# Optimization experiments

Hardware: AMD Instinct MI355X
Metric: run time of the kernel (lower is better)

The kernel has to match this reference:

```python
import jax, jax.numpy as jnp
import numpy as np
from jax import lax

B, N, H = 2048, 8192, 10  # batch, grid points, MLP hidden width (default NetworkStructure)
BETA = 0.1                # G(x) = 1 - exp(-beta*x)


def setup_inputs() -> dict:
    key = jax.random.key(0)
    ks = jax.random.split(key, 12)
    y_plus = jax.random.uniform(ks[0], (B, 1), dtype=jnp.float32) * 500.0
    i = jax.random.randint(ks[1], (B, 1), 0, N)
    DU_DY = jax.random.normal(ks[2], (B, 1, N), dtype=jnp.float32)
    # Y is a strictly increasing wall-normal grid per sample
    incr = jax.random.uniform(ks[3], (B, 1, N), dtype=jnp.float32) * 0.01 + 1e-4
    Y = jnp.cumsum(incr, axis=-1)
    s = 0.3
    # alphanet MLP (1 -> H -> 1)
    aw1 = jax.random.normal(ks[4], (1, H), dtype=jnp.float32) * s
    ab1 = jax.random.normal(ks[5], (H,), dtype=jnp.float32) * s
    aw2 = jax.random.normal(ks[6], (H, 1), dtype=jnp.float32) * s
    ab2 = jax.random.normal(ks[7], (1,), dtype=jnp.float32) * s
    # output MLP (1 -> H -> 1)
    w1 = jax.random.normal(ks[8], (1, H), dtype=jnp.float32) * s
    b1 = jax.random.normal(ks[9], (H,), dtype=jnp.float32) * s
    w2 = jax.random.normal(ks[10], (H, 1), dtype=jnp.float32) * s
    b2 = jax.random.normal(ks[11], (1,), dtype=jnp.float32) * s
    return {"y_plus": y_plus, "i": i, "DU_DY": DU_DY, "Y": Y,
            "aw1": aw1, "ab1": ab1, "aw2": aw2, "ab2": ab2,
            "w1": w1, "b1": b1, "w2": w2, "b2": b2}


def _mlp(x, w1, b1, w2, b2):
    return jax.nn.relu(x @ w1 + b1) @ w2 + b2


def _d_alpha_u(a, n, du, y):
    """Vectorized Caputo-style fractional derivative.
    a: [B] alpha in [0,1]; n: [B] int index; du, y: [B, N]."""
    yn = jnp.take_along_axis(y, n[:, None], axis=1)[:, 0]            # Y[n]
    t = (1.0 - a)[:, None]                                            # exponent 1-alpha
    k = jnp.arange(y.shape[1])
    mask = k[None, :] <= (n[:, None] - 2)                             # k = 0 .. n-2
    y_next = jnp.concatenate([y[:, 1:], y[:, -1:]], axis=1)          # Y[k+1]
    d0 = jnp.where(mask, yn[:, None] - y, 1.0)                        # guard neg bases
    d1 = jnp.where(mask, yn[:, None] - y_next, 1.0)
    bk = jnp.where(mask, d0 ** t - d1 ** t, 0.0)
    sum_main = jnp.sum(bk * du, axis=1)
    nm1 = jnp.clip(n - 1, 0)
    y_nm1 = jnp.take_along_axis(y, nm1[:, None], axis=1)[:, 0]
    du_nm1 = jnp.take_along_axis(du, nm1[:, None], axis=1)[:, 0]
    base = jnp.where(n >= 1, yn - y_nm1, 1.0)
    last = jnp.where(n >= 1, base ** t[:, 0] * du_nm1, 0.0)
    fac = jnp.exp(-lax.lgamma(2.0 - a))                               # 1/Gamma(2-a)
    frac = jnp.where(n == 0, 0.0, fac * (sum_main + last))
    # alpha == 0 branch: trapezoid integral of DU_DY up to index n
    seg = (y[:, 1:] - y[:, :-1]) * (du[:, 1:] + du[:, :-1]) * 0.5
    cum = jnp.concatenate([jnp.zeros((y.shape[0], 1), y.dtype), jnp.cumsum(seg, axis=1)], axis=1)
    trap = jnp.take_along_axis(cum, n[:, None], axis=1)[:, 0]
    # alpha == 1 branch: DU_DY[n]
    dun = jnp.take_along_axis(du, n[:, None], axis=1)[:, 0]
    return jnp.where(a == 0.0, trap, jnp.where(a == 1.0, dun, frac))


def reference(y_plus, i, DU_DY, Y, aw1, ab1, aw2, ab2, w1, b1, w2, b2):
    # AlphaNet with alpha0=1: alpha = 1 - sigmoid(mlp(y+)) * (1 - exp(-beta*y+))
    g = 1.0 - jnp.exp(-BETA * y_plus)
    alpha = 1.0 - jax.nn.sigmoid(_mlp(y_plus, aw1, ab1, aw2, ab2)) * g   # [B,1]
    a = alpha[:, 0]
    n = i[:, 0]
    du = DU_DY[:, 0, :]
    y = Y[:, 0, :]
    d = _d_alpha_u(a, n, du, y)[:, None]                                  # [B,1]
    return _mlp(d, w1, b1, w2, b2)
```

## Files before the change

kernel.cpp:

```cpp
#include <hip/hip_runtime.h>
#include <math.h>

#define BB 2048
#define NN 8192
#define HH 10
#define BETA 0.1f

__device__ __forceinline__ float fast_log2(float x) {
    float r; asm("v_log_f32 %0, %1" : "=v"(r) : "v"(x)); return r;
}
__device__ __forceinline__ float fast_exp2(float x) {
    float r; asm("v_exp_f32 %0, %1" : "=v"(r) : "v"(x)); return r;
}

__global__ __launch_bounds__(256) void frac_mlp_kernel(
    const float* __restrict__ y_plus,
    const int*   __restrict__ iidx,
    const float* __restrict__ DU,
    const float* __restrict__ Y,
    const float* __restrict__ aw1, const float* __restrict__ ab1,
    const float* __restrict__ aw2, const float* __restrict__ ab2,
    const float* __restrict__ w1,  const float* __restrict__ b1,
    const float* __restrict__ w2,  const float* __restrict__ b2,
    float* __restrict__ out)
{
    const int b   = blockIdx.x;
    const int tid = threadIdx.x;
    const int n   = iidx[b];
    const float yp = y_plus[b];

    float m = ab2[0];
    #pragma unroll
    for (int h = 0; h < HH; ++h)
        m += fmaxf(fmaf(yp, aw1[h], ab1[h]), 0.f) * aw2[h];
    const float g   = 1.f - expf(-BETA * yp);
    const float sig = 1.f / (1.f + expf(-m));
    const float a   = 1.f - sig * g;
    const float t   = 1.f - a;

    const float* yr = Y  + (size_t)b * NN;
    const float* dr = DU + (size_t)b * NN;
    const float yn = yr[n];

    double sm = 0.0;
    double tr = 0.0;

    const bool need_main = (a != 0.f) && (a != 1.f) && (n >= 2);
    const bool need_trap = (a == 0.f) && (n >= 1);

    if (need_main) {
        const int kend = n - 2;
        for (int k0 = tid * 8; k0 <= kend; k0 += 256 * 8) {
            float4 ya = *reinterpret_cast<const float4*>(yr + k0);
            float4 yb = *reinterpret_cast<const float4*>(yr + k0 + 4);
            float4 da = *reinterpret_cast<const float4*>(dr + k0);
            float4 db = *reinterpret_cast<const float4*>(dr + k0 + 4);
            float ynext = (k0 + 8 <= kend + 1) ? yr[k0 + 8] : yb.w;
            float yv[9] = {ya.x, ya.y, ya.z, ya.w, yb.x, yb.y, yb.z, yb.w, ynext};
            float dv[8] = {da.x, da.y, da.z, da.w, db.x, db.y, db.z, db.w};
            float p[9];
            #pragma unroll
            for (int j = 0; j < 9; ++j) {
                float x = fmaxf(yn - yv[j], 1e-30f);
                p[j] = fast_exp2(t * fast_log2(x));
            }
            float acc = 0.f;
            #pragma unroll
            for (int q = 0; q < 8; ++q) {
                if (k0 + q <= kend)
                    acc = fmaf(p[q] - p[q + 1], dv[q], acc);
            }
            sm += (double)acc;
        }
    }
    if (need_trap) {
        const int kend = n - 1;
        for (int k0 = tid * 4; k0 <= kend; k0 += 256 * 4) {
            float4 y4 = *reinterpret_cast<const float4*>(yr + k0);
            float4 d4 = *reinterpret_cast<const float4*>(dr + k0);
            float ynext = (k0 + 4 <= kend + 1) ? yr[k0 + 4] : y4.w;
            float dnext = (k0 + 4 <= kend + 1) ? dr[k0 + 4] : d4.w;
            float yv[5] = {y4.x, y4.y, y4.z, y4.w, ynext};
            float dv[5] = {d4.x, d4.y, d4.z, d4.w, dnext};
            float acc = 0.f;
            #pragma unroll
            for (int q = 0; q < 4; ++q) {
                int k = k0 + q;
                if (k <= kend)
                    acc += (yv[q + 1] - yv[q]) * (dv[q + 1] + dv[q]) * 0.5f;
            }
            tr += (double)acc;
        }
    }

    for (int off = 32; off > 0; off >>= 1) {
        sm += __shfl_down(sm, off, 64);
        tr += __shfl_down(tr, off, 64);
    }
    __shared__ double s_sm[4], s_tr[4];
    const int wave = tid >> 6, lane = tid & 63;
    if (lane == 0) { s_sm[wave] = sm; s_tr[wave] = tr; }
    __syncthreads();

    if (tid == 0) {
        double smT = s_sm[0] + s_sm[1] + s_sm[2] + s_sm[3];
        double trT = s_tr[0] + s_tr[1] + s_tr[2] + s_tr[3];
        float dres;
        if (a == 0.f) {
            dres = (float)trT;
        } else if (a == 1.f) {
            dres = dr[n];
        } else if (n == 0) {
            dres = 0.f;
        } else {
            float last = powf(yn - yr[n - 1], t) * dr[n - 1];
            float fac  = expf(-lgammaf(2.f - a));
            dres = fac * ((float)smT + last);
        }
        float o = b2[0];
        #pragma unroll
        for (int h = 0; h < HH; ++h)
            o += fmaxf(fmaf(dres, w1[h], b1[h]), 0.f) * w2[h];
        out[b] = o;
    }
}

extern "C" void kernel_launch(void* const* d_in, const int* in_sizes, int n_in,
                              void* d_out, int out_size, void* d_ws, size_t ws_size,
                              hipStream_t stream) {
    const float* y_plus = (const float*)d_in[0];
    const int*   iidx   = (const int*)  d_in[1];
    const float* DU     = (const float*)d_in[2];
    const float* Y      = (const float*)d_in[3];
    const float* aw1    = (const float*)d_in[4];
    const float* ab1    = (const float*)d_in[5];
    const float* aw2    = (const float*)d_in[6];
    const float* ab2    = (const float*)d_in[7];
    const float* w1     = (const float*)d_in[8];
    const float* b1     = (const float*)d_in[9];
    const float* w2     = (const float*)d_in[10];
    const float* b2     = (const float*)d_in[11];
    float* out = (float*)d_out;

    frac_mlp_kernel<<<BB, 256, 0, stream>>>(y_plus, iidx, DU, Y,
                                            aw1, ab1, aw2, ab2,
                                            w1, b1, w2, b2, out);
}
```

Baseline: 18.73 us.

## Split per-sample reduction across four blocks with a separate finalize kernel

Each sample's sum over up to 8192 grid points is now split across four blocks (a 2D grid). Each thread handles exactly one 8-element chunk and writes a double partial to workspace. A second small kernel adds the partials and runs the final MLP per sample. The aim is more parallelism and shorter per-block latency, at the cost of a second launch, workspace traffic, and blocks whose chunk lies past n and exit with almost no work.

```diff
diff --git a/kernel.cpp b/kernel.cpp
--- a/kernel.cpp
+++ b/kernel.cpp
@@ -5,6 +5,8 @@
 #define NN 8192
 #define HH 10
 #define BETA 0.1f
+#define CHUNK 2048
+#define NSPLIT 4
 
 __device__ __forceinline__ float fast_log2(float x) {
     float r; asm("v_log_f32 %0, %1" : "=v"(r) : "v"(x)); return r;
@@ -13,7 +15,105 @@
     float r; asm("v_exp_f32 %0, %1" : "=v"(r) : "v"(x)); return r;
 }
 
-__global__ __launch_bounds__(256) void frac_mlp_kernel(
+__device__ __forceinline__ float alpha_of(float yp,
+    const float* __restrict__ aw1, const float* __restrict__ ab1,
+    const float* __restrict__ aw2, const float* __restrict__ ab2) {
+    float m = ab2[0];
+    #pragma unroll
+    for (int h = 0; h < HH; ++h)
+        m += fmaxf(fmaf(yp, aw1[h], ab1[h]), 0.f) * aw2[h];
+    const float g   = 1.f - expf(-BETA * yp);
+    const float sig = 1.f / (1.f + expf(-m));
+    return 1.f - sig * g;
+}
+
+__global__ __launch_bounds__(256) void frac_partial_kernel(
+    const float* __restrict__ y_plus,
+    const int*   __restrict__ iidx,
+    const float* __restrict__ DU,
+    const float* __restrict__ Y,
+    const float* __restrict__ aw1, const float* __restrict__ ab1,
+    const float* __restrict__ aw2, const float* __restrict__ ab2,
+    double2* __restrict__ ws2)
+{
+    const int b   = blockIdx.x;
+    const int s   = blockIdx.y;
+    const int tid = threadIdx.x;
+    const int n   = iidx[b];
+
+    const float a = alpha_of(y_plus[b], aw1, ab1, aw2, ab2);
+    const float t = 1.f - a;
+
+    const float* yr = Y  + (size_t)b * NN;
+    const float* dr = DU + (size_t)b * NN;
+
+    const bool need_main = (a != 0.f) && (a != 1.f) && (n >= 2);
+    const bool need_trap = (a == 0.f) && (n >= 1);
+
+    float sm = 0.f;
+    float tr = 0.f;
+
+    if (need_main) {
+        const int kend = n - 2;
+        const int k0 = s * CHUNK + tid * 8;
+        if (k0 <= kend) {
+            float4 ya = *reinterpret_cast<const float4*>(yr + k0);
+            float4 yb = *reinterpret_cast<const float4*>(yr + k0 + 4);
+            float4 da = *reinterpret_cast<const float4*>(dr + k0);
+            float4 db = *reinterpret_cast<const float4*>(dr + k0 + 4);
+            float ynext = (k0 + 8 <= kend + 1) ? yr[k0 + 8] : yb.w;
+            const float yn = yr[n];
+            float yv[9] = {ya.x, ya.y, ya.z, ya.w, yb.x, yb.y, yb.z, yb.w, ynext};
+            float dv[8] = {da.x, da.y, da.z, da.w, db.x, db.y, db.z, db.w};
+            float p[9];
+            #pragma unroll
+            for (int j = 0; j < 9; ++j) {
+                float x = fmaxf(yn - yv[j], 1e-30f);
+                p[j] = fast_exp2(t * fast_log2(x));
+            }
+            #pragma unroll
+            for (int q = 0; q < 8; ++q)
+                if (k0 + q <= kend)
+                    sm = fmaf(p[q] - p[q + 1], dv[q], sm);
+        }
+    }
+    if (need_trap) {
+        const int kend = n - 1;
+        const int k0 = s * CHUNK + tid * 8;
+        if (k0 <= kend) {
+            float4 ya = *reinterpret_cast<const float4*>(yr + k0);
+            float4 yb = *reinterpret_cast<const float4*>(yr + k0 + 4);
+            float4 da = *reinterpret_cast<const float4*>(dr + k0);
+            float4 db = *reinterpret_cast<const float4*>(dr + k0 + 4);
+            float ynext = (k0 + 8 <= kend + 1) ? yr[k0 + 8] : yb.w;
+            float dnext = (k0 + 8 <= kend + 1) ? dr[k0 + 8] : db.w;
+            float yv[9] = {ya.x, ya.y, ya.z, ya.w, yb.x, yb.y, yb.z, yb.w, ynext};
+            float dv[9] = {da.x, da.y, da.z, da.w, db.x, db.y, db.z, db.w, dnext};
+            #pragma unroll
+            for (int q = 0; q < 8; ++q)
+                if (k0 + q <= kend)
+                    tr += (yv[q + 1] - yv[q]) * (dv[q + 1] + dv[q]) * 0.5f;
+        }
+    }
+
+    double smd = (double)sm, trd = (double)tr;
+    for (int off = 32; off > 0; off >>= 1) {
+        smd += __shfl_down(smd, off, 64);
+        trd += __shfl_down(trd, off, 64);
+    }
+    __shared__ double s_sm[4], s_tr[4];
+    const int wave = tid >> 6, lane = tid & 63;
+    if (lane == 0) { s_sm[wave] = smd; s_tr[wave] = trd; }
+    __syncthreads();
+    if (tid == 0) {
+        double2 r;
+        r.x = s_sm[0] + s_sm[1] + s_sm[2] + s_sm[3];
+        r.y = s_tr[0] + s_tr[1] + s_tr[2] + s_tr[3];
+        ws2[b * NSPLIT + s] = r;
+    }
+}
+
+__global__ __launch_bounds__(256) void frac_final_kernel(
     const float* __restrict__ y_plus,
     const int*   __restrict__ iidx,
     const float* __restrict__ DU,
@@ -22,107 +122,42 @@
     const float* __restrict__ aw2, const float* __restrict__ ab2,
     const float* __restrict__ w1,  const float* __restrict__ b1,
     const float* __restrict__ w2,  const float* __restrict__ b2,
+    const double2* __restrict__ ws2,
     float* __restrict__ out)
 {
-    const int b   = blockIdx.x;
-    const int tid = threadIdx.x;
-    const int n   = iidx[b];
-    const float yp = y_plus[b];
+    const int b = blockIdx.x * 256 + threadIdx.x;
+    if (b >= BB) return;
+    const int n = iidx[b];
+    const float a = alpha_of(y_plus[b], aw1, ab1, aw2, ab2);
+    const float t = 1.f - a;
 
-    float m = ab2[0];
+    double sm = 0.0, tr = 0.0;
     #pragma unroll
-    for (int h = 0; h < HH; ++h)
-        m += fmaxf(fmaf(yp, aw1[h], ab1[h]), 0.f) * aw2[h];
-    const float g   = 1.f - expf(-BETA * yp);
-    const float sig = 1.f / (1.f + expf(-m));
-    const float a   = 1.f - sig * g;
-    const float t   = 1.f - a;
+    for (int s = 0; s < NSPLIT; ++s) {
+        double2 r = ws2[b * NSPLIT + s];
+        sm += r.x; tr += r.y;
+    }
 
     const float* yr = Y  + (size_t)b * NN;
     const float* dr = DU + (size_t)b * NN;
-    const float yn = yr[n];
 
-    double sm = 0.0;
-    double tr = 0.0;
-
-    const bool need_main = (a != 0.f) && (a != 1.f) && (n >= 2);
-    const bool need_trap = (a == 0.f) && (n >= 1);
-
-    if (need_main) {
-        const int kend = n - 2;
-        for (int k0 = tid * 8; k0 <= kend; k0 += 256 * 8) {
-            float4 ya = *reinterpret_cast<const float4*>(yr + k0);
-            float4 yb = *reinterpret_cast<const float4*>(yr + k0 + 4);
-            float4 da = *reinterpret_cast<const float4*>(dr + k0);
-            float4 db = *reinterpret_cast<const float4*>(dr + k0 + 4);
-            float ynext = (k0 + 8 <= kend + 1) ? yr[k0 + 8] : yb.w;
-            float yv[9] = {ya.x, ya.y, ya.z, ya.w, yb.x, yb.y, yb.z, yb.w, ynext};
-            float dv[8] = {da.x, da.y, da.z, da.w, db.x, db.y, db.z, db.w};
-            float p[9];
-            #pragma unroll
-            for (int j = 0; j < 9; ++j) {
-                float x = fmaxf(yn - yv[j], 1e-30f);
-                p[j] = fast_exp2(t * fast_log2(x));
-            }
-            float acc = 0.f;
-            #pragma unroll
-            for (int q = 0; q < 8; ++q) {
-                if (k0 + q <= kend)
-                    acc = fmaf(p[q] - p[q + 1], dv[q], acc);
-            }
-            sm += (double)acc;
-        }
+    float dres;
+    if (a == 0.f) {
+        dres = (float)tr;
+    } else if (a == 1.f) {
+        dres = dr[n];
+    } else if (n == 0) {
+        dres = 0.f;
+    } else {
+        float last = powf(yr[n] - yr[n - 1], t) * dr[n - 1];
+        float fac  = expf(-lgammaf(2.f - a));
+        dres = fac * ((float)sm + last);
     }
-    if (need_trap) {
-        const int kend = n - 1;
-        for (int k0 = tid * 4; k0 <= kend; k0 += 256 * 4) {
-            float4 y4 = *reinterpret_cast<const float4*>(yr + k0);
-            float4 d4 = *reinterpret_cast<const float4*>(dr + k0);
-            float ynext = (k0 + 4 <= kend + 1) ? yr[k0 + 4] : y4.w;
-            float dnext = (k0 + 4 <= kend + 1) ? dr[k0 + 4] : d4.w;
-            float yv[5] = {y4.x, y4.y, y4.z, y4.w, ynext};
-            float dv[5] = {d4.x, d4.y, d4.z, d4.w, dnext};
-            float acc = 0.f;
-            #pragma unroll
-            for (int q = 0; q < 4; ++q) {
-                int k = k0 + q;
-                if (k <= kend)
-                    acc += (yv[q + 1] - yv[q]) * (dv[q + 1] + dv[q]) * 0.5f;
-            }
-            tr += (double)acc;
-        }
-    }
-
-    for (int off = 32; off > 0; off >>= 1) {
-        sm += __shfl_down(sm, off, 64);
-        tr += __shfl_down(tr, off, 64);
-    }
-    __shared__ double s_sm[4], s_tr[4];
-    const int wave = tid >> 6, lane = tid & 63;
-    if (lane == 0) { s_sm[wave] = sm; s_tr[wave] = tr; }
-    __syncthreads();
-
-    if (tid == 0) {
-        double smT = s_sm[0] + s_sm[1] + s_sm[2] + s_sm[3];
-        double trT = s_tr[0] + s_tr[1] + s_tr[2] + s_tr[3];
-        float dres;
-        if (a == 0.f) {
-            dres = (float)trT;
-        } else if (a == 1.f) {
-            dres = dr[n];
-        } else if (n == 0) {
-            dres = 0.f;
-        } else {
-            float last = powf(yn - yr[n - 1], t) * dr[n - 1];
-            float fac  = expf(-lgammaf(2.f - a));
-            dres = fac * ((float)smT + last);
-        }
-        float o = b2[0];
-        #pragma unroll
-        for (int h = 0; h < HH; ++h)
-            o += fmaxf(fmaf(dres, w1[h], b1[h]), 0.f) * w2[h];
-        out[b] = o;
-    }
+    float o = b2[0];
+    #pragma unroll
+    for (int h = 0; h < HH; ++h)
+        o += fmaxf(fmaf(dres, w1[h], b1[h]), 0.f) * w2[h];
+    out[b] = o;
 }
 
 extern "C" void kernel_launch(void* const* d_in, const int* in_sizes, int n_in,
@@ -141,8 +176,12 @@
     const float* w2     = (const float*)d_in[10];
     const float* b2     = (const float*)d_in[11];
     float* out = (float*)d_out;
+    double2* ws2 = (double2*)d_ws;
 
-    frac_mlp_kernel<<<BB, 256, 0, stream>>>(y_plus, iidx, DU, Y,
-                                            aw1, ab1, aw2, ab2,
-                                            w1, b1, w2, b2, out);
+    dim3 grid1(BB, NSPLIT);
+    frac_partial_kernel<<<grid1, 256, 0, stream>>>(y_plus, iidx, DU, Y,
+                                                   aw1, ab1, aw2, ab2, ws2);
+    frac_final_kernel<<<(BB + 255) / 256, 256, 0, stream>>>(y_plus, iidx, DU, Y,
+                                                            aw1, ab1, aw2, ab2,
+                                                            w1, b1, w2, b2, ws2, out);
 }
```

Measured after the change: 21.58 us. 1.15x slower.
